# Kernel tuning notes

Hardware: AMD Instinct MI355X
Metric: run time of the kernel (lower is better)

## Reference

```python
import jax, jax.numpy as jnp
import numpy as np

# ---- maxflat pyramid filters (pfilters('maxflat')) ----
def _maxflat_filters():
    sqrt2 = np.sqrt(2.0)
    M1 = M2 = 1.0 / sqrt2
    k1 = 1.0 - sqrt2
    k2 = k3 = M1
    h_half = np.array([0.25 * k2 * k3, 0.5 * k2, 1.0 + 0.5 * k2 * k3]) * M1
    h = np.concatenate([h_half, h_half[:-1][::-1]]) * sqrt2          # len 5
    g_half = np.array([-0.125 * k1 * k2 * k3,
                       0.25 * k1 * k2,
                       -0.5 * k1 - 0.5 * k3 - 0.375 * k1 * k2 * k3,
                       1.0 + 0.5 * k1 * k2]) * M2
    g = np.concatenate([g_half, g_half[:-1][::-1]]) * sqrt2          # len 7
    return h.astype(np.float32), g.astype(np.float32)

# highpass from g, as in wfb2dec: h1 = -g * (-1)**(arange(1,L+1)-c)
def _wfb_filters():
    h, g = _maxflat_filters()
    len_h1 = len(g)                      # 7 (odd)
    c = int(np.floor((len_h1 + 1.0) / 2.0))   # 4
    h1 = (-g * (-1.0) ** (np.arange(1, len_h1 + 1) - c)).astype(np.float32)
    ext_h0 = int(np.floor(len(h) / 2.0))      # 2
    ext_h1 = len_h1 - c + 1                   # 4
    return h, h1, ext_h0, ext_h1

# periodic row filtering along last axis (torch rowfiltering: periodic pad +
# cross-correlation, which F.conv2d / lax conv both compute without flip)
def rowfilt(x, f, ext1):
    L = f.shape[0]
    ext2 = L - ext1 - 1
    W = x.shape[-1]
    xe = jnp.concatenate([x[..., -ext1:], x, x[..., :ext2]], axis=-1)
    y = f[0] * xe[..., 0:W]
    for k in range(1, L):                 # tiny fixed tap loop, fuses fine
        y = y + f[k] * xe[..., k:k + W]
    return y

def colfilt(x, f, ext1):
    return jnp.swapaxes(rowfilt(jnp.swapaxes(x, -1, -2), f, ext1), -1, -2)


def setup_inputs() -> dict:
    key = jax.random.key(0)
    x = jax.random.normal(key, (8, 3, 1024, 1024), dtype=jnp.float32)
    return {"x": x}


def reference(x):
    # Pycontourlet.batch_multi_channel_pdfbdec with pfilt='maxflat',
    # nlevs=[0] -> wfb2dec path: one level of separable wavelet FB with
    # periodic extension; returns [xLL, [xLH, xHL, xHH]] (stacked here).
    h_np, h1_np, e0, e1 = _wfb_filters()
    h = jnp.asarray(h_np)
    h1 = jnp.asarray(h1_np)

    x_L = rowfilt(x, h, e0)[..., ::2]          # [B,C,H,W/2]
    x_H = rowfilt(x, h1, e1)[..., ::2]

    x_LL = colfilt(x_L, h, e0)[..., ::2, :]    # [B,C,H/2,W/2]
    x_LH = colfilt(x_L, h1, e1)[..., ::2, :]
    x_HL = colfilt(x_H, h, e0)[..., ::2, :]
    x_HH = colfilt(x_H, h1, e1)[..., ::2, :]

    return jnp.stack([x_LL, x_LH, x_HL, x_HH])  # [4,B,C,H/2,W/2]
```

## Files before the change

### kernel.cpp

```cpp
#include <hip/hip_runtime.h>


constexpr int H = 1024, W = 1024;
constexpr int NIMG = 24;
constexpr int HOUT = 512, WOUT = 512;
constexpr int TO = 32;
constexpr int RIN = 69;
constexpr int PAD = 36;

__global__ __launch_bounds__(256)
void wfb_kernel(const float* __restrict__ x, float* __restrict__ out) {
    __shared__ float s_L[RIN][PAD];
    __shared__ float s_H[RIN][PAD];

    const float h0c[5] = {0.125f, 0.35355339059327373f, 1.25f,
                          0.35355339059327373f, 0.125f};
    const float h1c[7] = {0.025888347648318447f,  0.07322330470336313f,
                          -0.06878156646177083f, -0.8535533905932737f,
                          -0.06878156646177083f,  0.07322330470336313f,
                          0.025888347648318447f};

    const int tid = threadIdx.x;
    const int img = blockIdx.z;
    const int r0 = blockIdx.y * TO;
    const int c0 = blockIdx.x * TO;
    const float* __restrict__ xin = x + (size_t)img * H * W;
    const int rbase = 2 * r0 - 4;
    const int cbase = 2 * c0 - 4;

    for (int m = tid; m < RIN * 4; m += 256) {
        int r = m >> 2;
        int g = m & 3;
        int gr = (rbase + r) & (H - 1);
        const float* __restrict__ rowp = xin + (size_t)gr * W;
        int b0 = cbase + 16 * g;
        float v[24];
        #pragma unroll
        for (int t = 0; t < 6; ++t) {
            int gc = (b0 + 4 * t) & (W - 1);
            float4 f = *(const float4*)(rowp + gc);
            v[4*t + 0] = f.x; v[4*t + 1] = f.y;
            v[4*t + 2] = f.z; v[4*t + 3] = f.w;
        }
        float Lo[8], Ho[8];
        #pragma unroll
        for (int u = 0; u < 8; ++u) {
            const float* p = v + 2 * u;
            Lo[u] = h0c[0]*p[2] + h0c[1]*p[3] + h0c[2]*p[4]
                  + h0c[3]*p[5] + h0c[4]*p[6];
            Ho[u] = h1c[0]*p[0] + h1c[1]*p[1] + h1c[2]*p[2] + h1c[3]*p[3]
                  + h1c[4]*p[4] + h1c[5]*p[5] + h1c[6]*p[6];
        }
        int j0 = 8 * g;
        *(float4*)&s_L[r][j0]     = make_float4(Lo[0], Lo[1], Lo[2], Lo[3]);
        *(float4*)&s_L[r][j0 + 4] = make_float4(Lo[4], Lo[5], Lo[6], Lo[7]);
        *(float4*)&s_H[r][j0]     = make_float4(Ho[0], Ho[1], Ho[2], Ho[3]);
        *(float4*)&s_H[r][j0 + 4] = make_float4(Ho[4], Ho[5], Ho[6], Ho[7]);
    }
    __syncthreads();

    constexpr size_t SB = (size_t)NIMG * HOUT * WOUT;
    float* __restrict__ o = out + (size_t)img * HOUT * WOUT;
    {
        int i  = tid >> 3;
        int jj = (tid & 7) * 4;
        float LLx=0,LLy=0,LLz=0,LLw=0, HLx=0,HLy=0,HLz=0,HLw=0;
        float LHx=0,LHy=0,LHz=0,LHw=0, HHx=0,HHy=0,HHz=0,HHw=0;
        #pragma unroll
        for (int k = 0; k < 5; ++k) {
            float4 a = *(const float4*)&s_L[2*i + 2 + k][jj];
            float4 b = *(const float4*)&s_H[2*i + 2 + k][jj];
            LLx += h0c[k]*a.x; LLy += h0c[k]*a.y; LLz += h0c[k]*a.z; LLw += h0c[k]*a.w;
            HLx += h0c[k]*b.x; HLy += h0c[k]*b.y; HLz += h0c[k]*b.z; HLw += h0c[k]*b.w;
        }
        #pragma unroll
        for (int k = 0; k < 7; ++k) {
            float4 a = *(const float4*)&s_L[2*i + k][jj];
            float4 b = *(const float4*)&s_H[2*i + k][jj];
            LHx += h1c[k]*a.x; LHy += h1c[k]*a.y; LHz += h1c[k]*a.z; LHw += h1c[k]*a.w;
            HHx += h1c[k]*b.x; HHy += h1c[k]*b.y; HHz += h1c[k]*b.z; HHw += h1c[k]*b.w;
        }
        size_t off = (size_t)(r0 + i) * WOUT + (c0 + jj);
        *(float4*)(o + 0 * SB + off) = make_float4(LLx, LLy, LLz, LLw);
        *(float4*)(o + 1 * SB + off) = make_float4(LHx, LHy, LHz, LHw);
        *(float4*)(o + 2 * SB + off) = make_float4(HLx, HLy, HLz, HLw);
        *(float4*)(o + 3 * SB + off) = make_float4(HHx, HHy, HHz, HHw);
    }
}

extern "C" void kernel_launch(void* const* d_in, const int* in_sizes, int n_in,
                              void* d_out, int out_size, void* d_ws, size_t ws_size,
                              hipStream_t stream) {
    const float* x = (const float*)d_in[0];
    float* out = (float*)d_out;
    dim3 grid(WOUT / TO, HOUT / TO, NIMG);
    wfb_kernel<<<grid, dim3(256), 0, stream>>>(x, out);
}
```

Measured before the change: 182.9 us.

## Process four column tiles per block with double-buffered LDS and register prefetch

Each block now handles four consecutive 32-wide output tiles instead of one. Global loads for the next tiles are issued into registers while the current tile's column filtering runs, and row-filter results alternate between two shared-memory buffers. The intent is to hide global load latency and spread per-block setup over more work. In exchange, the grid has four times fewer blocks, LDS use doubles, and register pressure rises, which may limit occupancy.

```diff
diff --git a/kernel.cpp b/kernel.cpp
--- a/kernel.cpp
+++ b/kernel.cpp
@@ -5,13 +5,15 @@
 constexpr int NIMG = 24;
 constexpr int HOUT = 512, WOUT = 512;
 constexpr int TO = 32;
+constexpr int NT = 4;
 constexpr int RIN = 69;
 constexpr int PAD = 36;
+constexpr int NITEM = RIN * 4;
 
-__global__ __launch_bounds__(256)
+__global__ __launch_bounds__(256, 4)
 void wfb_kernel(const float* __restrict__ x, float* __restrict__ out) {
-    __shared__ float s_L[RIN][PAD];
-    __shared__ float s_H[RIN][PAD];
+    __shared__ float s_L[2][RIN][PAD];
+    __shared__ float s_H[2][RIN][PAD];
 
     const float h0c[5] = {0.125f, 0.35355339059327373f, 1.25f,
                           0.35355339059327373f, 0.125f};
@@ -23,68 +25,121 @@
     const int tid = threadIdx.x;
     const int img = blockIdx.z;
     const int r0 = blockIdx.y * TO;
-    const int c0 = blockIdx.x * TO;
+    const int c0b = blockIdx.x * (NT * TO);
     const float* __restrict__ xin = x + (size_t)img * H * W;
     const int rbase = 2 * r0 - 4;
-    const int cbase = 2 * c0 - 4;
 
-    for (int m = tid; m < RIN * 4; m += 256) {
-        int r = m >> 2;
-        int g = m & 3;
-        int gr = (rbase + r) & (H - 1);
-        const float* __restrict__ rowp = xin + (size_t)gr * W;
-        int b0 = cbase + 16 * g;
-        float v[24];
-        #pragma unroll
-        for (int t = 0; t < 6; ++t) {
-            int gc = (b0 + 4 * t) & (W - 1);
-            float4 f = *(const float4*)(rowp + gc);
-            v[4*t + 0] = f.x; v[4*t + 1] = f.y;
-            v[4*t + 2] = f.z; v[4*t + 3] = f.w;
+    const int m0 = tid;
+    const int m1 = tid + 256;
+    const bool has1 = (m1 < NITEM);
+    const int r_0 = m0 >> 2, g_0 = m0 & 3;
+    const int r_1 = (has1 ? m1 : m0) >> 2, g_1 = (has1 ? m1 : m0) & 3;
+    const float* __restrict__ rowp0 = xin + (size_t)((rbase + r_0) & (H - 1)) * W;
+    const float* __restrict__ rowp1 = xin + (size_t)((rbase + r_1) & (H - 1)) * W;
+
+    float v0[24], v1[24];
+
+    auto LOAD = [&](int t) {
+        const int cbase = 2 * (c0b + t * TO) - 4;
+        {
+            const int b0 = cbase + 16 * g_0;
+            #pragma unroll
+            for (int q = 0; q < 6; ++q) {
+                int gc = (b0 + 4 * q) & (W - 1);
+                float4 f = *(const float4*)(rowp0 + gc);
+                v0[4*q+0] = f.x; v0[4*q+1] = f.y;
+                v0[4*q+2] = f.z; v0[4*q+3] = f.w;
+            }
         }
-        float Lo[8], Ho[8];
-        #pragma unroll
-        for (int u = 0; u < 8; ++u) {
-            const float* p = v + 2 * u;
-            Lo[u] = h0c[0]*p[2] + h0c[1]*p[3] + h0c[2]*p[4]
-                  + h0c[3]*p[5] + h0c[4]*p[6];
-            Ho[u] = h1c[0]*p[0] + h1c[1]*p[1] + h1c[2]*p[2] + h1c[3]*p[3]
-                  + h1c[4]*p[4] + h1c[5]*p[5] + h1c[6]*p[6];
+        if (has1) {
+            const int b0 = cbase + 16 * g_1;
+            #pragma unroll
+            for (int q = 0; q < 6; ++q) {
+                int gc = (b0 + 4 * q) & (W - 1);
+                float4 f = *(const float4*)(rowp1 + gc);
+                v1[4*q+0] = f.x; v1[4*q+1] = f.y;
+                v1[4*q+2] = f.z; v1[4*q+3] = f.w;
+            }
         }
-        int j0 = 8 * g;
-        *(float4*)&s_L[r][j0]     = make_float4(Lo[0], Lo[1], Lo[2], Lo[3]);
-        *(float4*)&s_L[r][j0 + 4] = make_float4(Lo[4], Lo[5], Lo[6], Lo[7]);
-        *(float4*)&s_H[r][j0]     = make_float4(Ho[0], Ho[1], Ho[2], Ho[3]);
-        *(float4*)&s_H[r][j0 + 4] = make_float4(Ho[4], Ho[5], Ho[6], Ho[7]);
-    }
-    __syncthreads();
+    };
+
+    auto ROWFILT = [&](int buf) {
+        {
+            float Lo[8], Ho[8];
+            #pragma unroll
+            for (int u = 0; u < 8; ++u) {
+                const float* p = v0 + 2 * u;
+                Lo[u] = h0c[0]*p[2] + h0c[1]*p[3] + h0c[2]*p[4]
+                      + h0c[3]*p[5] + h0c[4]*p[6];
+                Ho[u] = h1c[0]*p[0] + h1c[1]*p[1] + h1c[2]*p[2] + h1c[3]*p[3]
+                      + h1c[4]*p[4] + h1c[5]*p[5] + h1c[6]*p[6];
+            }
+            const int j0 = 8 * g_0;
+            *(float4*)&s_L[buf][r_0][j0]     = make_float4(Lo[0],Lo[1],Lo[2],Lo[3]);
+            *(float4*)&s_L[buf][r_0][j0 + 4] = make_float4(Lo[4],Lo[5],Lo[6],Lo[7]);
+            *(float4*)&s_H[buf][r_0][j0]     = make_float4(Ho[0],Ho[1],Ho[2],Ho[3]);
+            *(float4*)&s_H[buf][r_0][j0 + 4] = make_float4(Ho[4],Ho[5],Ho[6],Ho[7]);
+        }
+        if (has1) {
+            float Lo[8], Ho[8];
+            #pragma unroll
+            for (int u = 0; u < 8; ++u) {
+                const float* p = v1 + 2 * u;
+                Lo[u] = h0c[0]*p[2] + h0c[1]*p[3] + h0c[2]*p[4]
+                      + h0c[3]*p[5] + h0c[4]*p[6];
+                Ho[u] = h1c[0]*p[0] + h1c[1]*p[1] + h1c[2]*p[2] + h1c[3]*p[3]
+                      + h1c[4]*p[4] + h1c[5]*p[5] + h1c[6]*p[6];
+            }
+            const int j0 = 8 * g_1;
+            *(float4*)&s_L[buf][r_1][j0]     = make_float4(Lo[0],Lo[1],Lo[2],Lo[3]);
+            *(float4*)&s_L[buf][r_1][j0 + 4] = make_float4(Lo[4],Lo[5],Lo[6],Lo[7]);
+            *(float4*)&s_H[buf][r_1][j0]     = make_float4(Ho[0],Ho[1],Ho[2],Ho[3]);
+            *(float4*)&s_H[buf][r_1][j0 + 4] = make_float4(Ho[4],Ho[5],Ho[6],Ho[7]);
+        }
+    };
 
     constexpr size_t SB = (size_t)NIMG * HOUT * WOUT;
     float* __restrict__ o = out + (size_t)img * HOUT * WOUT;
-    {
-        int i  = tid >> 3;
-        int jj = (tid & 7) * 4;
+    const int i_  = tid >> 3;
+    const int jj_ = (tid & 7) * 4;
+
+    auto PHASE2 = [&](int t) {
+        const int buf = t & 1;
+        const int c0 = c0b + t * TO;
         float LLx=0,LLy=0,LLz=0,LLw=0, HLx=0,HLy=0,HLz=0,HLw=0;
         float LHx=0,LHy=0,LHz=0,LHw=0, HHx=0,HHy=0,HHz=0,HHw=0;
         #pragma unroll
         for (int k = 0; k < 5; ++k) {
-            float4 a = *(const float4*)&s_L[2*i + 2 + k][jj];
-            float4 b = *(const float4*)&s_H[2*i + 2 + k][jj];
+            float4 a = *(const float4*)&s_L[buf][2*i_ + 2 + k][jj_];
+            float4 b = *(const float4*)&s_H[buf][2*i_ + 2 + k][jj_];
             LLx += h0c[k]*a.x; LLy += h0c[k]*a.y; LLz += h0c[k]*a.z; LLw += h0c[k]*a.w;
             HLx += h0c[k]*b.x; HLy += h0c[k]*b.y; HLz += h0c[k]*b.z; HLw += h0c[k]*b.w;
         }
         #pragma unroll
         for (int k = 0; k < 7; ++k) {
-            float4 a = *(const float4*)&s_L[2*i + k][jj];
-            float4 b = *(const float4*)&s_H[2*i + k][jj];
+            float4 a = *(const float4*)&s_L[buf][2*i_ + k][jj_];
+            float4 b = *(const float4*)&s_H[buf][2*i_ + k][jj_];
             LHx += h1c[k]*a.x; LHy += h1c[k]*a.y; LHz += h1c[k]*a.z; LHw += h1c[k]*a.w;
             HHx += h1c[k]*b.x; HHy += h1c[k]*b.y; HHz += h1c[k]*b.z; HHw += h1c[k]*b.w;
         }
-        size_t off = (size_t)(r0 + i) * WOUT + (c0 + jj);
+        size_t off = (size_t)(r0 + i_) * WOUT + (c0 + jj_);
         *(float4*)(o + 0 * SB + off) = make_float4(LLx, LLy, LLz, LLw);
         *(float4*)(o + 1 * SB + off) = make_float4(LHx, LHy, LHz, LHw);
         *(float4*)(o + 2 * SB + off) = make_float4(HLx, HLy, HLz, HLw);
         *(float4*)(o + 3 * SB + off) = make_float4(HHx, HHy, HHz, HHw);
+    };
+
+    LOAD(0);
+    ROWFILT(0);
+    LOAD(1);
+    __syncthreads();
+
+    #pragma unroll
+    for (int t = 0; t < NT; ++t) {
+        if (t + 1 < NT) ROWFILT((t + 1) & 1);
+        if (t + 2 < NT) LOAD(t + 2);
+        PHASE2(t);
+        if (t + 1 < NT) __syncthreads();
     }
 }
 
@@ -93,6 +148,6 @@
                               hipStream_t stream) {
     const float* x = (const float*)d_in[0];
     float* out = (float*)d_out;
-    dim3 grid(WOUT / TO, HOUT / TO, NIMG);
+    dim3 grid(WOUT / (TO * NT), HOUT / TO, NIMG);
     wfb_kernel<<<grid, dim3(256), 0, stream>>>(x, out);
 }
```

Measured after the change: 189.8 us. 1.04x slower.

## Compute all four subbands per thread from registers, dropping shared memory

Applied to the files above, without the earlier changes.

Removes the shared-memory tile and block barrier. Each thread now loads the 7 input rows it needs directly from global memory, applies both row filters, and accumulates the column filters in registers, with loads double-buffered across two register arrays. This removes LDS traffic and synchronisation, but every input row is now read by about 3.5 threads instead of once per block, so the kernel depends on L1/L2 caching to absorb the extra global reads. It also raises register pressure.

```diff
diff --git a/kernel.cpp b/kernel.cpp
--- a/kernel.cpp
+++ b/kernel.cpp
@@ -4,15 +4,11 @@
 constexpr int H = 1024, W = 1024;
 constexpr int NIMG = 24;
 constexpr int HOUT = 512, WOUT = 512;
-constexpr int TO = 32;
-constexpr int RIN = 69;
-constexpr int PAD = 36;
+constexpr int BROWS = 32;
+constexpr int BCOLS = 64;
 
 __global__ __launch_bounds__(256)
 void wfb_kernel(const float* __restrict__ x, float* __restrict__ out) {
-    __shared__ float s_L[RIN][PAD];
-    __shared__ float s_H[RIN][PAD];
-
     const float h0c[5] = {0.125f, 0.35355339059327373f, 1.25f,
                           0.35355339059327373f, 0.125f};
     const float h1c[7] = {0.025888347648318447f,  0.07322330470336313f,
@@ -22,70 +18,67 @@
 
     const int tid = threadIdx.x;
     const int img = blockIdx.z;
-    const int r0 = blockIdx.y * TO;
-    const int c0 = blockIdx.x * TO;
+    const int R  = blockIdx.y * BROWS + (tid >> 3);
+    const int J0 = blockIdx.x * BCOLS + (tid & 7) * 8;
     const float* __restrict__ xin = x + (size_t)img * H * W;
-    const int rbase = 2 * r0 - 4;
-    const int cbase = 2 * c0 - 4;
 
-    for (int m = tid; m < RIN * 4; m += 256) {
-        int r = m >> 2;
-        int g = m & 3;
-        int gr = (rbase + r) & (H - 1);
+    const int rb = 2 * R - 4;
+    const int cb = 2 * J0 - 4;
+
+    float LL[8] = {0,0,0,0,0,0,0,0}, LH[8] = {0,0,0,0,0,0,0,0};
+    float HL[8] = {0,0,0,0,0,0,0,0}, HH[8] = {0,0,0,0,0,0,0,0};
+
+    auto LOADROW = [&](int d, float* v) {
+        const int gr = (rb + d) & (H - 1);
         const float* __restrict__ rowp = xin + (size_t)gr * W;
-        int b0 = cbase + 16 * g;
-        float v[24];
         #pragma unroll
-        for (int t = 0; t < 6; ++t) {
-            int gc = (b0 + 4 * t) & (W - 1);
+        for (int q = 0; q < 6; ++q) {
+            int gc = (cb + 4 * q) & (W - 1);
             float4 f = *(const float4*)(rowp + gc);
-            v[4*t + 0] = f.x; v[4*t + 1] = f.y;
-            v[4*t + 2] = f.z; v[4*t + 3] = f.w;
+            v[4*q + 0] = f.x; v[4*q + 1] = f.y;
+            v[4*q + 2] = f.z; v[4*q + 3] = f.w;
         }
-        float Lo[8], Ho[8];
+    };
+
+    auto STEP = [&](int d, const float* v) {
         #pragma unroll
         for (int u = 0; u < 8; ++u) {
             const float* p = v + 2 * u;
-            Lo[u] = h0c[0]*p[2] + h0c[1]*p[3] + h0c[2]*p[4]
-                  + h0c[3]*p[5] + h0c[4]*p[6];
-            Ho[u] = h1c[0]*p[0] + h1c[1]*p[1] + h1c[2]*p[2] + h1c[3]*p[3]
-                  + h1c[4]*p[4] + h1c[5]*p[5] + h1c[6]*p[6];
+            float Lr = h0c[0]*p[2] + h0c[1]*p[3] + h0c[2]*p[4]
+                     + h0c[3]*p[5] + h0c[4]*p[6];
+            float Hr = h1c[0]*p[0] + h1c[1]*p[1] + h1c[2]*p[2] + h1c[3]*p[3]
+                     + h1c[4]*p[4] + h1c[5]*p[5] + h1c[6]*p[6];
+            LH[u] += h1c[d] * Lr;
+            HH[u] += h1c[d] * Hr;
+            if (d >= 2) {
+                LL[u] += h0c[d-2] * Lr;
+                HL[u] += h0c[d-2] * Hr;
+            }
         }
-        int j0 = 8 * g;
-        *(float4*)&s_L[r][j0]     = make_float4(Lo[0], Lo[1], Lo[2], Lo[3]);
-        *(float4*)&s_L[r][j0 + 4] = make_float4(Lo[4], Lo[5], Lo[6], Lo[7]);
-        *(float4*)&s_H[r][j0]     = make_float4(Ho[0], Ho[1], Ho[2], Ho[3]);
-        *(float4*)&s_H[r][j0 + 4] = make_float4(Ho[4], Ho[5], Ho[6], Ho[7]);
-    }
-    __syncthreads();
+    };
+
+    float va[24], vb[24];
+    LOADROW(0, va);
+    LOADROW(1, vb);
+    STEP(0, va);  LOADROW(2, va);
+    STEP(1, vb);  LOADROW(3, vb);
+    STEP(2, va);  LOADROW(4, va);
+    STEP(3, vb);  LOADROW(5, vb);
+    STEP(4, va);  LOADROW(6, va);
+    STEP(5, vb);
+    STEP(6, va);
 
     constexpr size_t SB = (size_t)NIMG * HOUT * WOUT;
     float* __restrict__ o = out + (size_t)img * HOUT * WOUT;
-    {
-        int i  = tid >> 3;
-        int jj = (tid & 7) * 4;
-        float LLx=0,LLy=0,LLz=0,LLw=0, HLx=0,HLy=0,HLz=0,HLw=0;
-        float LHx=0,LHy=0,LHz=0,LHw=0, HHx=0,HHy=0,HHz=0,HHw=0;
-        #pragma unroll
-        for (int k = 0; k < 5; ++k) {
-            float4 a = *(const float4*)&s_L[2*i + 2 + k][jj];
-            float4 b = *(const float4*)&s_H[2*i + 2 + k][jj];
-            LLx += h0c[k]*a.x; LLy += h0c[k]*a.y; LLz += h0c[k]*a.z; LLw += h0c[k]*a.w;
-            HLx += h0c[k]*b.x; HLy += h0c[k]*b.y; HLz += h0c[k]*b.z; HLw += h0c[k]*b.w;
-        }
-        #pragma unroll
-        for (int k = 0; k < 7; ++k) {
-            float4 a = *(const float4*)&s_L[2*i + k][jj];
-            float4 b = *(const float4*)&s_H[2*i + k][jj];
-            LHx += h1c[k]*a.x; LHy += h1c[k]*a.y; LHz += h1c[k]*a.z; LHw += h1c[k]*a.w;
-            HHx += h1c[k]*b.x; HHy += h1c[k]*b.y; HHz += h1c[k]*b.z; HHw += h1c[k]*b.w;
-        }
-        size_t off = (size_t)(r0 + i) * WOUT + (c0 + jj);
-        *(float4*)(o + 0 * SB + off) = make_float4(LLx, LLy, LLz, LLw);
-        *(float4*)(o + 1 * SB + off) = make_float4(LHx, LHy, LHz, LHw);
-        *(float4*)(o + 2 * SB + off) = make_float4(HLx, HLy, HLz, HLw);
-        *(float4*)(o + 3 * SB + off) = make_float4(HHx, HHy, HHz, HHw);
-    }
+    const size_t off = (size_t)R * WOUT + J0;
+    *(float4*)(o + 0*SB + off)     = make_float4(LL[0], LL[1], LL[2], LL[3]);
+    *(float4*)(o + 0*SB + off + 4) = make_float4(LL[4], LL[5], LL[6], LL[7]);
+    *(float4*)(o + 1*SB + off)     = make_float4(LH[0], LH[1], LH[2], LH[3]);
+    *(float4*)(o + 1*SB + off + 4) = make_float4(LH[4], LH[5], LH[6], LH[7]);
+    *(float4*)(o + 2*SB + off)     = make_float4(HL[0], HL[1], HL[2], HL[3]);
+    *(float4*)(o + 2*SB + off + 4) = make_float4(HL[4], HL[5], HL[6], HL[7]);
+    *(float4*)(o + 3*SB + off)     = make_float4(HH[0], HH[1], HH[2], HH[3]);
+    *(float4*)(o + 3*SB + off + 4) = make_float4(HH[4], HH[5], HH[6], HH[7]);
 }
 
 extern "C" void kernel_launch(void* const* d_in, const int* in_sizes, int n_in,
@@ -93,6 +86,6 @@
                               hipStream_t stream) {
     const float* x = (const float*)d_in[0];
     float* out = (float*)d_out;
-    dim3 grid(WOUT / TO, HOUT / TO, NIMG);
+    dim3 grid(WOUT / BCOLS, HOUT / BROWS, NIMG);
     wfb_kernel<<<grid, dim3(256), 0, stream>>>(x, out);
 }
```

Result: slower. 205.1 us (+12.2%).
